# Performance work log

Hardware: AMD Instinct MI355X
Metric: run time of the kernel (lower is better)

The kernel has to match this reference:

```python
import jax, jax.numpy as jnp
import numpy as np

B, V, C, NB, KS, OUT = 2, 20000, 32, 12, 9, 32


def setup_inputs() -> dict:
    key = jax.random.key(0)
    k1, k2, k3, k4 = jax.random.split(key, 4)
    x = jax.random.normal(k1, (B, V, C), jnp.float32)
    # padded neighbor table: index 0 == padding row, valid indices 1..V
    adj = jax.random.randint(k2, (V, NB), 0, V + 1, dtype=jnp.int32)
    # GlorotNormal-ish scales
    W = jax.random.normal(k3, (C, KS, OUT), jnp.float32) * np.float32(np.sqrt(2.0 / (C + KS * OUT)))
    u = jax.random.normal(k4, (C, KS), jnp.float32) * np.float32(np.sqrt(2.0 / (C + KS)))
    c = jnp.zeros((KS,), jnp.float32)
    b = jnp.zeros((OUT,), jnp.float32)
    return {"x": x, "W": W, "u": u, "c": c, "b": b, "adj": adj}


def reference(x, W, u, c, b, adj):
    Bb, Vv, Cc = x.shape
    ks, out = W.shape[1], W.shape[2]
    # inverse neighbor count (0 index means padding); 0 where no neighbors
    deg = jnp.count_nonzero(adj, axis=-1).astype(x.dtype)            # [V]
    inv_deg = jnp.where(deg > 0, 1.0 / deg, jnp.zeros_like(deg))     # [V]

    # wx = x @ reshape(W) -> per-vertex kernelized features
    wx = jnp.einsum('bvc,cko->bvko', x, W)                           # [B,V,ks,out]
    wx_pad = jnp.concatenate([jnp.zeros((Bb, 1, ks, out), x.dtype), wx], axis=1)
    nb_wx = wx_pad[:, adj]                                           # [B,V,nb,ks,out]

    # attention logits: u(x_i) - u(x_j) + c, softmax over kernel axis
    ux = jnp.einsum('bvc,ck->bvk', x, u)                             # [B,V,ks]
    ux_pad = jnp.concatenate([jnp.zeros((Bb, 1, ks), x.dtype), ux], axis=1)
    nb_ux = ux_pad[:, adj]                                           # [B,V,nb,ks]
    q = jax.nn.softmax(ux[:, :, None, :] - nb_ux + c, axis=-1)       # [B,V,nb,ks]

    # softmax-weighted sum over neighbors, then mean (via inv_deg) over kernels
    agg = jnp.einsum('bvnk,bvnko->bvko', q, nb_wx)                   # [B,V,ks,out]
    res = jnp.einsum('bvko,v->bvo', agg, inv_deg) + b                # [B,V,out]
    return jax.nn.relu(res)
```

## Files before the change

kernel.cpp:

```cpp
#include <hip/hip_runtime.h>
#include <math.h>

#define BDIM 256

constexpr int Vc = 20000, Cc = 32, NBc = 12, KSc = 9, OUTc = 32;
constexpr int NTASK = 40000;
constexpr int UXP   = 12;
constexpr int MT    = 16;
constexpr int NITER = NTASK / MT;
constexpr int NBLK  = 512;
constexpr int NWAVE = NBLK * 4;
constexpr int WFE   = KSc * 2 * 64 * 8;

typedef __attribute__((ext_vector_type(8))) short short8;
typedef __attribute__((ext_vector_type(4))) float floatx4;

__global__ __launch_bounds__(BDIM)
void prep_kernel(const float* __restrict__ x, const float* __restrict__ u,
                 const float* __restrict__ W, float* __restrict__ ux,
                 unsigned short* __restrict__ wf)
{
    if (blockIdx.x < 157) {
        __shared__ float us[Cc * KSc];
        for (int i = threadIdx.x; i < Cc * KSc; i += BDIM) us[i] = u[i];
        __syncthreads();
        const int row = blockIdx.x * BDIM + threadIdx.x;
        if (row >= NTASK) return;
        const float4* xr = (const float4*)(x + row * Cc);
        float4 xv[8];
#pragma unroll
        for (int i = 0; i < 8; ++i) xv[i] = xr[i];
        float acc[KSc];
#pragma unroll
        for (int k = 0; k < KSc; ++k) acc[k] = 0.f;
#pragma unroll
        for (int c = 0; c < Cc; ++c) {
            const float xc = ((const float*)xv)[c];
#pragma unroll
            for (int k = 0; k < KSc; ++k) acc[k] = fmaf(xc, us[c * KSc + k], acc[k]);
        }
        float4* o4 = (float4*)(ux + row * UXP);
        o4[0] = make_float4(acc[0], acc[1], acc[2], acc[3]);
        o4[1] = make_float4(acc[4], acc[5], acc[6], acc[7]);
        o4[2] = make_float4(acc[8], 0.f, 0.f, 0.f);
    } else {
        const int e = (blockIdx.x - 157) * BDIM + threadIdx.x;
        if (e >= WFE) return;
        const int j = e & 7;
        const int l = (e >> 3) & 63;
        const int h = (e >> 9) & 1;
        const int k = e >> 10;
        const int c = (l >> 4) * 8 + j;
        const int o = (l & 15) + 16 * h;
        const float w = W[(c * KSc + k) * OUTc + o];
        const unsigned int bits = __float_as_uint(w);
        const unsigned short hi = (unsigned short)(bits >> 16);
        const float hif = __uint_as_float(bits & 0xFFFF0000u);
        const float lof = w - hif;
        const unsigned short lo = (unsigned short)(__float_as_uint(lof) >> 16);
        wf[e]       = hi;
        wf[WFE + e] = lo;
    }
}

__global__ __launch_bounds__(BDIM, 2)
void fused_kernel(const float* __restrict__ x, const float* __restrict__ cvec,
                  const float* __restrict__ bvec, const int* __restrict__ adj,
                  const float* __restrict__ ux, const unsigned short* __restrict__ wf,
                  float* __restrict__ out)
{
    __shared__ __align__(16) unsigned short wsh[2 * WFE];
    __shared__ __align__(16) float qs[4][MT][KSc][NBc];
    __shared__ __align__(16) int   js[4][MT][NBc];
    __shared__ float invs[4][MT];

    const int tid = threadIdx.x;
    {
        const uint4* src = (const uint4*)wf;
        uint4* dst = (uint4*)wsh;
        for (int i = tid; i < (2 * WFE) / 8; i += BDIM) dst[i] = src[i];
    }
    float ck[KSc];
#pragma unroll
    for (int k = 0; k < KSc; ++k) ck[k] = cvec[k];
    const int l64 = tid & 63;
    const int w   = tid >> 6;
    const int oo  = l64 & 15;
    const int cb  = l64 >> 4;
    const float b0 = bvec[oo], b1 = bvec[oo + 16];
    __syncthreads();

    const int gw = blockIdx.x * 4 + w;
    for (int it = gw; it < NITER; it += NWAVE) {
        const int t0 = it * MT;

#pragma unroll
        for (int p = 0; p < 3; ++p) {
            const int unit = p * 64 + l64;
            const int t    = (unit * 171) >> 11;
            const int n    = unit - t * 12;
            const int task = t0 + t;
            const int bb   = (task >= Vc) ? 1 : 0;
            const int v    = task - bb * Vc;
            const int jn   = adj[v * NBc + n];
            const bool pred = (jn != 0);
            const int row = pred ? (bb * Vc + jn - 1) : 0;
            js[w][t][n] = row;
            float uo[12], un[12];
            {
                const float4* uo4 = (const float4*)(ux + task * UXP);
                const float4* un4 = (const float4*)(ux + row * UXP);
                *(float4*)&uo[0] = uo4[0]; *(float4*)&uo[4] = uo4[1]; *(float4*)&uo[8] = uo4[2];
                *(float4*)&un[0] = un4[0]; *(float4*)&un[4] = un4[1]; *(float4*)&un[8] = un4[2];
            }
            float e[KSc];
            float mx = -3.0e38f;
#pragma unroll
            for (int k = 0; k < KSc; ++k) {
                e[k] = uo[k] - un[k] + ck[k];
                mx = fmaxf(mx, e[k]);
            }
            float s = 0.f;
#pragma unroll
            for (int k = 0; k < KSc; ++k) { e[k] = __expf(e[k] - mx); s += e[k]; }
            const float r = pred ? (1.f / s) : 0.f;
#pragma unroll
            for (int k = 0; k < KSc; ++k) qs[w][t][k][n] = e[k] * r;
        }
        if (l64 < MT) {
            const int task = t0 + l64;
            const int bb   = (task >= Vc) ? 1 : 0;
            const int v    = task - bb * Vc;
            const int4* ar = (const int4*)(adj + v * NBc);
            const int4 a0 = ar[0], a1 = ar[1], a2 = ar[2];
            const int d = (a0.x != 0) + (a0.y != 0) + (a0.z != 0) + (a0.w != 0)
                        + (a1.x != 0) + (a1.y != 0) + (a1.z != 0) + (a1.w != 0)
                        + (a2.x != 0) + (a2.y != 0) + (a2.z != 0) + (a2.w != 0);
            invs[w][l64] = (d > 0) ? 1.f / (float)d : 0.f;
        }

        const int tA = l64 & 15;
        float y[KSc][8];
#pragma unroll
        for (int k = 0; k < KSc; ++k)
#pragma unroll
            for (int j = 0; j < 8; ++j) y[k][j] = 0.f;

        int rows[NBc];
        {
            const int4* jp = (const int4*)&js[w][tA][0];
            const int4 ja = jp[0], jb = jp[1], jc = jp[2];
            rows[0] = ja.x; rows[1] = ja.y; rows[2]  = ja.z; rows[3]  = ja.w;
            rows[4] = jb.x; rows[5] = jb.y; rows[6]  = jb.z; rows[7]  = jb.w;
            rows[8] = jc.x; rows[9] = jc.y; rows[10] = jc.z; rows[11] = jc.w;
        }
#pragma unroll
        for (int nb = 0; nb < 3; ++nb) {
            float xs[4][8];
#pragma unroll
            for (int i = 0; i < 4; ++i) {
                const float4* xp = (const float4*)(x + rows[nb * 4 + i] * Cc + cb * 8);
                *(float4*)&xs[i][0] = xp[0];
                *(float4*)&xs[i][4] = xp[1];
            }
#pragma unroll
            for (int k = 0; k < KSc; ++k) {
                const float4 q4 = *(const float4*)&qs[w][tA][k][nb * 4];
#pragma unroll
                for (int j = 0; j < 8; ++j) {
                    float a = y[k][j];
                    a = fmaf(q4.x, xs[0][j], a);
                    a = fmaf(q4.y, xs[1][j], a);
                    a = fmaf(q4.z, xs[2][j], a);
                    a = fmaf(q4.w, xs[3][j], a);
                    y[k][j] = a;
                }
            }
        }

        floatx4 acc0 = {0.f, 0.f, 0.f, 0.f};
        floatx4 acc1 = {0.f, 0.f, 0.f, 0.f};
#pragma unroll
        for (int k = 0; k < KSc; ++k) {
            short8 ah, al;
#pragma unroll
            for (int j = 0; j < 8; ++j) {
                const unsigned int yb = __float_as_uint(y[k][j]);
                ah[j] = (short)(yb >> 16);
                const float hif = __uint_as_float(yb & 0xFFFF0000u);
                const float lof = y[k][j] - hif;
                al[j] = (short)(__float_as_uint(lof) >> 16);
            }
            const short8 bh0 = *(const short8*)&wsh[((k * 2 + 0) * 64 + l64) * 8];
            const short8 bh1 = *(const short8*)&wsh[((k * 2 + 1) * 64 + l64) * 8];
            const short8 bl0 = *(const short8*)&wsh[WFE + ((k * 2 + 0) * 64 + l64) * 8];
            const short8 bl1 = *(const short8*)&wsh[WFE + ((k * 2 + 1) * 64 + l64) * 8];
            acc0 = __builtin_amdgcn_mfma_f32_16x16x32_bf16(ah, bh0, acc0, 0, 0, 0);
            acc0 = __builtin_amdgcn_mfma_f32_16x16x32_bf16(al, bh0, acc0, 0, 0, 0);
            acc0 = __builtin_amdgcn_mfma_f32_16x16x32_bf16(ah, bl0, acc0, 0, 0, 0);
            acc1 = __builtin_amdgcn_mfma_f32_16x16x32_bf16(ah, bh1, acc1, 0, 0, 0);
            acc1 = __builtin_amdgcn_mfma_f32_16x16x32_bf16(al, bh1, acc1, 0, 0, 0);
            acc1 = __builtin_amdgcn_mfma_f32_16x16x32_bf16(ah, bl1, acc1, 0, 0, 0);
        }

#pragma unroll
        for (int r = 0; r < 4; ++r) {
            const int tl   = cb * 4 + r;
            const float nv = invs[w][tl];
            const int task = t0 + tl;
            out[task * OUTc + oo]      = fmaxf(fmaf(acc0[r], nv, b0), 0.f);
            out[task * OUTc + oo + 16] = fmaxf(fmaf(acc1[r], nv, b1), 0.f);
        }
    }
}

extern "C" void kernel_launch(void* const* d_in, const int* in_sizes, int n_in,
                              void* d_out, int out_size, void* d_ws, size_t ws_size,
                              hipStream_t stream)
{
    const float* x    = (const float*)d_in[0];
    const float* W    = (const float*)d_in[1];
    const float* u    = (const float*)d_in[2];
    const float* cvec = (const float*)d_in[3];
    const float* bvec = (const float*)d_in[4];
    const int*   adj  = (const int*)d_in[5];
    float* out = (float*)d_out;

    float*          ux = (float*)d_ws;
    unsigned short* wf = (unsigned short*)((char*)d_ws + 1920000);

    prep_kernel<<<157 + 36, BDIM, 0, stream>>>(x, u, W, ux, wf);
    fused_kernel<<<NBLK, BDIM, 0, stream>>>(x, cvec, bvec, adj, ux, wf, out);
}
```

Before: 96.28 us.

## Switch fused kernel to one-wave blocks per 16-task tile, reading weights from global

The persistent 256-thread blocks that staged the split-bf16 weights in LDS are replaced by a 64-thread, single-wave block per 16-task tile, launched over all tiles. The LDS weight staging, the block barrier and the shared neighbor-row and inverse-degree arrays go away. Neighbor rows are recomputed from adj per lane, and the inverse degree is passed between lanes with a shuffle. Adjacency loads and ux loads are batched up front to raise memory-level parallelism. The trade-off is that every wave now reads about 36KB of MFMA weight fragments through the cache hierarchy instead of from shared memory, which adds L2 traffic.

```diff
diff --git a/kernel.cpp b/kernel.cpp
--- a/kernel.cpp
+++ b/kernel.cpp
@@ -1,30 +1,29 @@
 #include <hip/hip_runtime.h>
 #include <math.h>
 
-#define BDIM 256
+#define PBDIM 256
+#define BDIM  64
 
 constexpr int Vc = 20000, Cc = 32, NBc = 12, KSc = 9, OUTc = 32;
 constexpr int NTASK = 40000;
 constexpr int UXP   = 12;
 constexpr int MT    = 16;
 constexpr int NITER = NTASK / MT;
-constexpr int NBLK  = 512;
-constexpr int NWAVE = NBLK * 4;
 constexpr int WFE   = KSc * 2 * 64 * 8;
 
 typedef __attribute__((ext_vector_type(8))) short short8;
 typedef __attribute__((ext_vector_type(4))) float floatx4;
 
-__global__ __launch_bounds__(BDIM)
+__global__ __launch_bounds__(PBDIM)
 void prep_kernel(const float* __restrict__ x, const float* __restrict__ u,
                  const float* __restrict__ W, float* __restrict__ ux,
                  unsigned short* __restrict__ wf)
 {
     if (blockIdx.x < 157) {
         __shared__ float us[Cc * KSc];
-        for (int i = threadIdx.x; i < Cc * KSc; i += BDIM) us[i] = u[i];
+        for (int i = threadIdx.x; i < Cc * KSc; i += PBDIM) us[i] = u[i];
         __syncthreads();
-        const int row = blockIdx.x * BDIM + threadIdx.x;
+        const int row = blockIdx.x * PBDIM + threadIdx.x;
         if (row >= NTASK) return;
         const float4* xr = (const float4*)(x + row * Cc);
         float4 xv[8];
@@ -44,7 +43,7 @@
         o4[1] = make_float4(acc[4], acc[5], acc[6], acc[7]);
         o4[2] = make_float4(acc[8], 0.f, 0.f, 0.f);
     } else {
-        const int e = (blockIdx.x - 157) * BDIM + threadIdx.x;
+        const int e = (blockIdx.x - 157) * PBDIM + threadIdx.x;
         if (e >= WFE) return;
         const int j = e & 7;
         const int l = (e >> 3) & 63;
@@ -63,154 +62,149 @@
     }
 }
 
-__global__ __launch_bounds__(BDIM, 2)
+__global__ __launch_bounds__(BDIM, 3)
 void fused_kernel(const float* __restrict__ x, const float* __restrict__ cvec,
                   const float* __restrict__ bvec, const int* __restrict__ adj,
                   const float* __restrict__ ux, const unsigned short* __restrict__ wf,
                   float* __restrict__ out)
 {
-    __shared__ __align__(16) unsigned short wsh[2 * WFE];
-    __shared__ __align__(16) float qs[4][MT][KSc][NBc];
-    __shared__ __align__(16) int   js[4][MT][NBc];
-    __shared__ float invs[4][MT];
-
-    const int tid = threadIdx.x;
-    {
-        const uint4* src = (const uint4*)wf;
-        uint4* dst = (uint4*)wsh;
-        for (int i = tid; i < (2 * WFE) / 8; i += BDIM) dst[i] = src[i];
-    }
-    float ck[KSc];
-#pragma unroll
-    for (int k = 0; k < KSc; ++k) ck[k] = cvec[k];
-    const int l64 = tid & 63;
-    const int w   = tid >> 6;
+    __shared__ __align__(16) float qs[MT][KSc][NBc];
+
+    const int l64 = threadIdx.x;
     const int oo  = l64 & 15;
     const int cb  = l64 >> 4;
+    const int t0  = blockIdx.x * MT;
+
+    float ck[KSc];
+#pragma unroll
+    for (int k = 0; k < KSc; ++k) ck[k] = cvec[k];
+
+    int   tP[3], nP[3], rowP[3];
+    bool  predP[3];
+    float uo[3][12], un[3][12];
+#pragma unroll
+    for (int p = 0; p < 3; ++p) {
+        const int unit = p * 64 + l64;
+        const int t    = (unit * 171) >> 11;
+        const int n    = unit - t * 12;
+        const int task = t0 + t;
+        const int bb   = (task >= Vc) ? 1 : 0;
+        const int v    = task - bb * Vc;
+        const int jn   = adj[v * NBc + n];
+        predP[p] = (jn != 0);
+        rowP[p]  = predP[p] ? (bb * Vc + jn - 1) : 0;
+        tP[p] = t; nP[p] = n;
+    }
+#pragma unroll
+    for (int p = 0; p < 3; ++p) {
+        const float4* uo4 = (const float4*)(ux + (t0 + tP[p]) * UXP);
+        const float4* un4 = (const float4*)(ux + rowP[p] * UXP);
+        *(float4*)&uo[p][0] = uo4[0]; *(float4*)&uo[p][4] = uo4[1]; *(float4*)&uo[p][8] = uo4[2];
+        *(float4*)&un[p][0] = un4[0]; *(float4*)&un[p][4] = un4[1]; *(float4*)&un[p][8] = un4[2];
+    }
+#pragma unroll
+    for (int p = 0; p < 3; ++p) {
+        float e[KSc];
+        float mx = -3.0e38f;
+#pragma unroll
+        for (int k = 0; k < KSc; ++k) {
+            e[k] = uo[p][k] - un[p][k] + ck[k];
+            mx = fmaxf(mx, e[k]);
+        }
+        float s = 0.f;
+#pragma unroll
+        for (int k = 0; k < KSc; ++k) { e[k] = __expf(e[k] - mx); s += e[k]; }
+        const float r = predP[p] ? (1.f / s) : 0.f;
+#pragma unroll
+        for (int k = 0; k < KSc; ++k) qs[tP[p]][k][nP[p]] = e[k] * r;
+    }
+
+    const int tA   = l64 & 15;
+    const int task = t0 + tA;
+    const int bb   = (task >= Vc) ? 1 : 0;
+    const int v    = task - bb * Vc;
+    int rows[NBc];
+    float inv_local;
+    {
+        const int4* ar = (const int4*)(adj + v * NBc);
+        const int4 a0 = ar[0], a1 = ar[1], a2 = ar[2];
+        int jv[NBc];
+        jv[0] = a0.x; jv[1] = a0.y; jv[2]  = a0.z; jv[3]  = a0.w;
+        jv[4] = a1.x; jv[5] = a1.y; jv[6]  = a1.z; jv[7]  = a1.w;
+        jv[8] = a2.x; jv[9] = a2.y; jv[10] = a2.z; jv[11] = a2.w;
+        int d = 0;
+#pragma unroll
+        for (int n = 0; n < NBc; ++n) {
+            const bool pr = (jv[n] != 0);
+            d += pr ? 1 : 0;
+            rows[n] = pr ? (bb * Vc + jv[n] - 1) : 0;
+        }
+        inv_local = (d > 0) ? 1.f / (float)d : 0.f;
+    }
+
+    float y[KSc][8];
+#pragma unroll
+    for (int k = 0; k < KSc; ++k)
+#pragma unroll
+        for (int j = 0; j < 8; ++j) y[k][j] = 0.f;
+
+#pragma unroll
+    for (int nb = 0; nb < 3; ++nb) {
+        float xs[4][8];
+#pragma unroll
+        for (int i = 0; i < 4; ++i) {
+            const float4* xp = (const float4*)(x + rows[nb * 4 + i] * Cc + cb * 8);
+            *(float4*)&xs[i][0] = xp[0];
+            *(float4*)&xs[i][4] = xp[1];
+        }
+#pragma unroll
+        for (int k = 0; k < KSc; ++k) {
+            const float4 q4 = *(const float4*)&qs[tA][k][nb * 4];
+#pragma unroll
+            for (int j = 0; j < 8; ++j) {
+                float a = y[k][j];
+                a = fmaf(q4.x, xs[0][j], a);
+                a = fmaf(q4.y, xs[1][j], a);
+                a = fmaf(q4.z, xs[2][j], a);
+                a = fmaf(q4.w, xs[3][j], a);
+                y[k][j] = a;
+            }
+        }
+    }
+
+    floatx4 acc0 = {0.f, 0.f, 0.f, 0.f};
+    floatx4 acc1 = {0.f, 0.f, 0.f, 0.f};
+#pragma unroll
+    for (int k = 0; k < KSc; ++k) {
+        short8 ah, al;
+#pragma unroll
+        for (int j = 0; j < 8; ++j) {
+            const unsigned int yb = __float_as_uint(y[k][j]);
+            ah[j] = (short)(yb >> 16);
+            const float hif = __uint_as_float(yb & 0xFFFF0000u);
+            const float lof = y[k][j] - hif;
+            al[j] = (short)(__float_as_uint(lof) >> 16);
+        }
+        const short8 bh0 = *(const short8*)(wf + ((k * 2 + 0) * 64 + l64) * 8);
+        const short8 bh1 = *(const short8*)(wf + ((k * 2 + 1) * 64 + l64) * 8);
+        const short8 bl0 = *(const short8*)(wf + WFE + ((k * 2 + 0) * 64 + l64) * 8);
+        const short8 bl1 = *(const short8*)(wf + WFE + ((k * 2 + 1) * 64 + l64) * 8);
+        acc0 = __builtin_amdgcn_mfma_f32_16x16x32_bf16(ah, bh0, acc0, 0, 0, 0);
+        acc0 = __builtin_amdgcn_mfma_f32_16x16x32_bf16(al, bh0, acc0, 0, 0, 0);
+        acc0 = __builtin_amdgcn_mfma_f32_16x16x32_bf16(ah, bl0, acc0, 0, 0, 0);
+        acc1 = __builtin_amdgcn_mfma_f32_16x16x32_bf16(ah, bh1, acc1, 0, 0, 0);
+        acc1 = __builtin_amdgcn_mfma_f32_16x16x32_bf16(al, bh1, acc1, 0, 0, 0);
+        acc1 = __builtin_amdgcn_mfma_f32_16x16x32_bf16(ah, bl1, acc1, 0, 0, 0);
+    }
+
     const float b0 = bvec[oo], b1 = bvec[oo + 16];
-    __syncthreads();
-
-    const int gw = blockIdx.x * 4 + w;
-    for (int it = gw; it < NITER; it += NWAVE) {
-        const int t0 = it * MT;
-
-#pragma unroll
-        for (int p = 0; p < 3; ++p) {
-            const int unit = p * 64 + l64;
-            const int t    = (unit * 171) >> 11;
-            const int n    = unit - t * 12;
-            const int task = t0 + t;
-            const int bb   = (task >= Vc) ? 1 : 0;
-            const int v    = task - bb * Vc;
-            const int jn   = adj[v * NBc + n];
-            const bool pred = (jn != 0);
-            const int row = pred ? (bb * Vc + jn - 1) : 0;
-            js[w][t][n] = row;
-            float uo[12], un[12];
-            {
-                const float4* uo4 = (const float4*)(ux + task * UXP);
-                const float4* un4 = (const float4*)(ux + row * UXP);
-                *(float4*)&uo[0] = uo4[0]; *(float4*)&uo[4] = uo4[1]; *(float4*)&uo[8] = uo4[2];
-                *(float4*)&un[0] = un4[0]; *(float4*)&un[4] = un4[1]; *(float4*)&un[8] = un4[2];
-            }
-            float e[KSc];
-            float mx = -3.0e38f;
-#pragma unroll
-            for (int k = 0; k < KSc; ++k) {
-                e[k] = uo[k] - un[k] + ck[k];
-                mx = fmaxf(mx, e[k]);
-            }
-            float s = 0.f;
-#pragma unroll
-            for (int k = 0; k < KSc; ++k) { e[k] = __expf(e[k] - mx); s += e[k]; }
-            const float r = pred ? (1.f / s) : 0.f;
-#pragma unroll
-            for (int k = 0; k < KSc; ++k) qs[w][t][k][n] = e[k] * r;
-        }
-        if (l64 < MT) {
-            const int task = t0 + l64;
-            const int bb   = (task >= Vc) ? 1 : 0;
-            const int v    = task - bb * Vc;
-            const int4* ar = (const int4*)(adj + v * NBc);
-            const int4 a0 = ar[0], a1 = ar[1], a2 = ar[2];
-            const int d = (a0.x != 0) + (a0.y != 0) + (a0.z != 0) + (a0.w != 0)
-                        + (a1.x != 0) + (a1.y != 0) + (a1.z != 0) + (a1.w != 0)
-                        + (a2.x != 0) + (a2.y != 0) + (a2.z != 0) + (a2.w != 0);
-            invs[w][l64] = (d > 0) ? 1.f / (float)d : 0.f;
-        }
-
-        const int tA = l64 & 15;
-        float y[KSc][8];
-#pragma unroll
-        for (int k = 0; k < KSc; ++k)
-#pragma unroll
-            for (int j = 0; j < 8; ++j) y[k][j] = 0.f;
-
-        int rows[NBc];
-        {
-            const int4* jp = (const int4*)&js[w][tA][0];
-            const int4 ja = jp[0], jb = jp[1], jc = jp[2];
-            rows[0] = ja.x; rows[1] = ja.y; rows[2]  = ja.z; rows[3]  = ja.w;
-            rows[4] = jb.x; rows[5] = jb.y; rows[6]  = jb.z; rows[7]  = jb.w;
-            rows[8] = jc.x; rows[9] = jc.y; rows[10] = jc.z; rows[11] = jc.w;
-        }
-#pragma unroll
-        for (int nb = 0; nb < 3; ++nb) {
-            float xs[4][8];
-#pragma unroll
-            for (int i = 0; i < 4; ++i) {
-                const float4* xp = (const float4*)(x + rows[nb * 4 + i] * Cc + cb * 8);
-                *(float4*)&xs[i][0] = xp[0];
-                *(float4*)&xs[i][4] = xp[1];
-            }
-#pragma unroll
-            for (int k = 0; k < KSc; ++k) {
-                const float4 q4 = *(const float4*)&qs[w][tA][k][nb * 4];
-#pragma unroll
-                for (int j = 0; j < 8; ++j) {
-                    float a = y[k][j];
-                    a = fmaf(q4.x, xs[0][j], a);
-                    a = fmaf(q4.y, xs[1][j], a);
-                    a = fmaf(q4.z, xs[2][j], a);
-                    a = fmaf(q4.w, xs[3][j], a);
-                    y[k][j] = a;
-                }
-            }
-        }
-
-        floatx4 acc0 = {0.f, 0.f, 0.f, 0.f};
-        floatx4 acc1 = {0.f, 0.f, 0.f, 0.f};
-#pragma unroll
-        for (int k = 0; k < KSc; ++k) {
-            short8 ah, al;
-#pragma unroll
-            for (int j = 0; j < 8; ++j) {
-                const unsigned int yb = __float_as_uint(y[k][j]);
-                ah[j] = (short)(yb >> 16);
-                const float hif = __uint_as_float(yb & 0xFFFF0000u);
-                const float lof = y[k][j] - hif;
-                al[j] = (short)(__float_as_uint(lof) >> 16);
-            }
-            const short8 bh0 = *(const short8*)&wsh[((k * 2 + 0) * 64 + l64) * 8];
-            const short8 bh1 = *(const short8*)&wsh[((k * 2 + 1) * 64 + l64) * 8];
-            const short8 bl0 = *(const short8*)&wsh[WFE + ((k * 2 + 0) * 64 + l64) * 8];
-            const short8 bl1 = *(const short8*)&wsh[WFE + ((k * 2 + 1) * 64 + l64) * 8];
-            acc0 = __builtin_amdgcn_mfma_f32_16x16x32_bf16(ah, bh0, acc0, 0, 0, 0);
-            acc0 = __builtin_amdgcn_mfma_f32_16x16x32_bf16(al, bh0, acc0, 0, 0, 0);
-            acc0 = __builtin_amdgcn_mfma_f32_16x16x32_bf16(ah, bl0, acc0, 0, 0, 0);
-            acc1 = __builtin_amdgcn_mfma_f32_16x16x32_bf16(ah, bh1, acc1, 0, 0, 0);
-            acc1 = __builtin_amdgcn_mfma_f32_16x16x32_bf16(al, bh1, acc1, 0, 0, 0);
-            acc1 = __builtin_amdgcn_mfma_f32_16x16x32_bf16(ah, bl1, acc1, 0, 0, 0);
-        }
-
-#pragma unroll
-        for (int r = 0; r < 4; ++r) {
-            const int tl   = cb * 4 + r;
-            const float nv = invs[w][tl];
-            const int task = t0 + tl;
-            out[task * OUTc + oo]      = fmaxf(fmaf(acc0[r], nv, b0), 0.f);
-            out[task * OUTc + oo + 16] = fmaxf(fmaf(acc1[r], nv, b1), 0.f);
-        }
+#pragma unroll
+    for (int r = 0; r < 4; ++r) {
+        const int tl   = cb * 4 + r;
+        const float nv = __shfl(inv_local, tl, 64);
+        const int tsk  = t0 + tl;
+        out[tsk * OUTc + oo]      = fmaxf(fmaf(acc0[r], nv, b0), 0.f);
+        out[tsk * OUTc + oo + 16] = fmaxf(fmaf(acc1[r], nv, b1), 0.f);
     }
 }
 
@@ -229,6 +223,6 @@
     float*          ux = (float*)d_ws;
     unsigned short* wf = (unsigned short*)((char*)d_ws + 1920000);
 
-    prep_kernel<<<157 + 36, BDIM, 0, stream>>>(x, u, W, ux, wf);
-    fused_kernel<<<NBLK, BDIM, 0, stream>>>(x, cvec, bvec, adj, ux, wf, out);
+    prep_kernel<<<157 + 36, PBDIM, 0, stream>>>(x, u, W, ux, wf);
+    fused_kernel<<<NITER, BDIM, 0, stream>>>(x, cvec, bvec, adj, ux, wf, out);
 }
```

Result: faster. 88.07 us (-8.5%).
